# Kernel optimization log

Hardware: AMD Instinct MI355X
Metric: run time of the kernel (lower is better)

The kernel has to match this reference:

```python
import jax, jax.numpy as jnp
import numpy as np

V, D, T, L, H = 32000, 1024, 2048, 2, 16
HS = D // H  # per-head dim (head_size // nheads)
FF = 4 * D
EPS = 1e-5


def _ln(x, g, b):
    m = jnp.mean(x, axis=-1, keepdims=True)
    v = jnp.mean((x - m) ** 2, axis=-1, keepdims=True)
    return (x - m) * jax.lax.rsqrt(v + EPS) * g + b


def setup_inputs() -> dict:
    key = jax.random.key(0)
    ks = jax.random.split(key, 16)
    s = lambda k, shape, fan: jax.random.normal(k, shape, jnp.float32) * (fan ** -0.5)
    return {
        "inputs": jax.random.randint(ks[0], (1, T), 0, V, dtype=jnp.int64),
        "tok_emb": s(ks[1], (V, D), D),
        "pos_emb": s(ks[2], (T, D), D),
        "ln1_g": jnp.ones((L, D)), "ln1_b": jnp.zeros((L, D)),
        "wq": s(ks[3], (L, H, D, HS), D),
        "wk": s(ks[4], (L, H, D, HS), D),
        "wv": s(ks[5], (L, H, D, HS), D),
        "ln2_g": jnp.ones((L, D)), "ln2_b": jnp.zeros((L, D)),
        "w1": s(ks[6], (L, D, FF), D), "b1": jnp.zeros((L, FF)),
        "w2": s(ks[7], (L, FF, D), FF), "b2": jnp.zeros((L, D)),
        "lnf_g": jnp.ones((D,)), "lnf_b": jnp.zeros((D,)),
        "w_un": s(ks[8], (D, V), D), "b_un": jnp.zeros((V,)),
    }


def reference(inputs, tok_emb, pos_emb, ln1_g, ln1_b, wq, wk, wv,
              ln2_g, ln2_b, w1, b1, w2, b2, lnf_g, lnf_b, w_un, b_un):
    b, t = inputs.shape
    x = tok_emb[inputs] + pos_emb[:t]  # [B,T,D]
    mask = jnp.tril(jnp.ones((t, t), dtype=bool))
    scale = jnp.asarray(D, x.dtype) ** -0.5  # source scales by x.shape[-1]**-0.5
    neg_inf = jnp.asarray(-jnp.inf, x.dtype)
    for l in range(L):
        h = _ln(x, ln1_g[l], ln1_b[l])
        q = jnp.einsum('btc,hcs->bhts', h, wq[l])
        k = jnp.einsum('btc,hcs->bhts', h, wk[l])
        v = jnp.einsum('btc,hcs->bhts', h, wv[l])
        scores = jnp.einsum('bhts,bhus->bhtu', q, k) * scale  # [B,H,T,T]
        scores = jnp.where(mask, scores, neg_inf)
        p = jax.nn.softmax(scores, axis=-1)
        att = jnp.einsum('bhtu,bhus->bhts', p, v)  # [B,H,T,HS]
        att = att.transpose(0, 2, 1, 3).reshape(b, t, H * HS)
        x = x + att
        h = _ln(x, ln2_g[l], ln2_b[l])
        h = jax.nn.relu(h @ w1[l] + b1[l]) @ w2[l] + b2[l]
        x = x + h
    x = _ln(x, lnf_g, lnf_b)
    return x @ w_un + b_un  # [B,T,V]
```

## Files before the change

### kernel.cpp

```cpp
#include <hip/hip_runtime.h>
#include <hip/hip_bf16.h>

#define TT 2048
#define DD 1024
#define NH 16
#define HSZ 64
#define FFD 4096
#define VV 32000
#define NL 2

typedef __bf16 bf16x8 __attribute__((ext_vector_type(8)));
typedef float f32x4 __attribute__((ext_vector_type(4)));

__device__ __forceinline__ unsigned short f2bf(float f) {
    unsigned int u = __float_as_uint(f);
    return (unsigned short)((u + 0x7FFFu + ((u >> 16) & 1u)) >> 16);
}

#define GLL(gsrc, ldst) \
  __builtin_amdgcn_global_load_lds((const __attribute__((address_space(1))) void*)(gsrc), \
                                   (__attribute__((address_space(3))) void*)(ldst), 16, 0, 0)

#define SWZ64(L)  ((L) ^ ((((L) >> 7) & 3) << 4))
#define SWZ128(L) ((L) ^ ((((L) >> 7) & 7) << 4))

#define VMW(n) asm volatile("s_waitcnt vmcnt(" #n ")" ::: "memory")

__global__ __launch_bounds__(256) void embed_kernel(
    const int* __restrict__ idx, const float* __restrict__ tok,
    const float* __restrict__ pos, float* __restrict__ x)
{
    int t = blockIdx.x;
    int d4 = threadIdx.x * 4;
    int token = idx[t];
    float4 a = *(const float4*)&tok[(size_t)token * DD + d4];
    float4 p = *(const float4*)&pos[(size_t)t * DD + d4];
    float4 r;
    r.x = a.x + p.x; r.y = a.y + p.y; r.z = a.z + p.z; r.w = a.w + p.w;
    *(float4*)&x[(size_t)t * DD + d4] = r;
}

__global__ __launch_bounds__(256) void ln_kernel(
    const float* __restrict__ x, const float* __restrict__ g,
    const float* __restrict__ b, unsigned short* __restrict__ out)
{
    int t = blockIdx.x;
    int tid = threadIdx.x;
    int d4 = tid * 4;
    float4 xv = *(const float4*)&x[(size_t)t * DD + d4];
    float s  = xv.x + xv.y + xv.z + xv.w;
    float s2 = xv.x*xv.x + xv.y*xv.y + xv.z*xv.z + xv.w*xv.w;
    #pragma unroll
    for (int off = 32; off >= 1; off >>= 1) {
        s  += __shfl_xor(s,  off);
        s2 += __shfl_xor(s2, off);
    }
    __shared__ float ls[4], ls2[4];
    int w = tid >> 6;
    if ((tid & 63) == 0) { ls[w] = s; ls2[w] = s2; }
    __syncthreads();
    float sum  = ls[0] + ls[1] + ls[2] + ls[3];
    float sum2 = ls2[0] + ls2[1] + ls2[2] + ls2[3];
    float mean = sum * (1.0f / DD);
    float var  = sum2 * (1.0f / DD) - mean * mean;
    float r = rsqrtf(var + 1e-5f);
    float4 gv = *(const float4*)&g[d4];
    float4 bv = *(const float4*)&b[d4];
    ushort4 pk;
    pk.x = f2bf((xv.x - mean) * r * gv.x + bv.x);
    pk.y = f2bf((xv.y - mean) * r * gv.y + bv.y);
    pk.z = f2bf((xv.z - mean) * r * gv.z + bv.z);
    pk.w = f2bf((xv.w - mean) * r * gv.w + bv.w);
    *(ushort4*)&out[(size_t)t * DD + d4] = pk;
}

__global__ __launch_bounds__(256) void tcast(
    const float* __restrict__ src, unsigned short* __restrict__ dst,
    int R, int C, size_t sstride, size_t dstride)
{
    __shared__ float tile[64][65];
    const float* s = src + (size_t)blockIdx.z * sstride;
    unsigned short* d = dst + (size_t)blockIdx.z * dstride;
    int c0 = blockIdx.x * 64, r0 = blockIdx.y * 64;
    #pragma unroll
    for (int i = 0; i < 16; ++i) {
        int id = i * 256 + threadIdx.x;
        int rr = id >> 6, cc = id & 63;
        tile[rr][cc] = s[(size_t)(r0 + rr) * C + (c0 + cc)];
    }
    __syncthreads();
    #pragma unroll
    for (int i = 0; i < 16; ++i) {
        int id = i * 256 + threadIdx.x;
        int cc = id >> 6, rr = id & 63;
        d[(size_t)(c0 + cc) * R + (r0 + rr)] = f2bf(tile[rr][cc]);
    }
}

__global__ __launch_bounds__(256) void qkv_tcast(
    const float* __restrict__ wq, const float* __restrict__ wk,
    const float* __restrict__ wv, unsigned short* __restrict__ dst)
{
    __shared__ float tile[64][65];
    int l = blockIdx.z;
    int mat = blockIdx.y >> 4, hh = blockIdx.y & 15;
    const float* s = (mat == 0) ? wq : (mat == 1) ? wk : wv;
    s += (((size_t)l * NH + hh) * DD) * HSZ;
    int r0 = blockIdx.x * 64;
    #pragma unroll
    for (int i = 0; i < 16; ++i) {
        int id = i * 256 + threadIdx.x;
        int rr = id >> 6, cc = id & 63;
        tile[rr][cc] = s[(size_t)(r0 + rr) * HSZ + cc];
    }
    __syncthreads();
    unsigned short* d = dst + (size_t)l * 3072 * DD + ((size_t)mat * DD + hh * HSZ) * DD;
    #pragma unroll
    for (int i = 0; i < 16; ++i) {
        int id = i * 256 + threadIdx.x;
        int cc = id >> 6, rr = id & 63;
        d[(size_t)cc * DD + (r0 + rr)] = f2bf(tile[rr][cc]);
    }
}

template<int EPI, int BN>
__global__ __launch_bounds__(256) void mgemm(
    const unsigned short* __restrict__ A, const unsigned short* __restrict__ Bt,
    const float* __restrict__ bias, void* __restrict__ outp,
    int M, int N, int K)
{
    constexpr int FN = BN / 64 * 2;
    __shared__ unsigned short As[3][128 * 32];
    __shared__ unsigned short Bs[3][BN * 32];
    int tid = threadIdx.x;
    int w = tid >> 6, lane = tid & 63;
    int l15 = lane & 15, l4 = lane >> 4;
    int bm = blockIdx.y * 128, bn = blockIdx.x * BN;
    int wr = (w >> 1) * 64, wc = (w & 1) * (BN / 2);

    f32x4 zz = {0.f, 0.f, 0.f, 0.f};
    f32x4 acc[4][FN];
    #pragma unroll
    for (int m = 0; m < 4; ++m)
        #pragma unroll
        for (int n = 0; n < FN; ++n) acc[m][n] = zz;

    int t16 = tid * 16;
    int lg = SWZ64(t16);
    int srow = lg >> 6;
    int skel = (lg & 63) >> 1;
    const unsigned short* aS0 = A + (size_t)(bm + srow) * K + skel;
    const unsigned short* aS1 = A + (size_t)(bm + 64 + srow) * K + skel;
    const unsigned short* bS0 = Bt + (size_t)(bn + srow) * K + skel;
    const unsigned short* bS1 = Bt + (size_t)(bn + 64 + srow) * K + skel;

    #define STAGE(t, slot) do { int kk_ = (t) * 32; \
        GLL(aS0 + kk_, (char*)As[slot] + w * 1024); \
        GLL(aS1 + kk_, (char*)As[slot] + 4096 + w * 1024); \
        GLL(bS0 + kk_, (char*)Bs[slot] + w * 1024); \
        if (BN == 128) GLL(bS1 + kk_, (char*)Bs[slot] + 4096 + w * 1024); } while (0)

    int aoff[4], boff[FN];
    #pragma unroll
    for (int m = 0; m < 4; ++m)
        aoff[m] = SWZ64((wr + m * 16 + l15) * 64 + l4 * 16);
    #pragma unroll
    for (int n = 0; n < FN; ++n)
        boff[n] = SWZ64((wc + n * 16 + l15) * 64 + l4 * 16);

    int nt = K >> 5;
    STAGE(0, 0);
    STAGE(1, 1);
    STAGE(2, 2);
    int slot = 0;
    for (int t = 0; t < nt; ++t) {
        if (BN == 128) {
            if (t + 2 < nt)      VMW(8);
            else if (t + 1 < nt) VMW(4);
            else                 VMW(0);
        } else {
            if (t + 2 < nt)      VMW(6);
            else if (t + 1 < nt) VMW(3);
            else                 VMW(0);
        }
        __builtin_amdgcn_sched_barrier(0);
        __builtin_amdgcn_s_barrier();
        __builtin_amdgcn_sched_barrier(0);
        bf16x8 af[4], bfr[FN];
        #pragma unroll
        for (int m = 0; m < 4; ++m) af[m] = *(const bf16x8*)((const char*)As[slot] + aoff[m]);
        #pragma unroll
        for (int n = 0; n < FN; ++n) bfr[n] = *(const bf16x8*)((const char*)Bs[slot] + boff[n]);
        #pragma unroll
        for (int m = 0; m < 4; ++m)
            #pragma unroll
            for (int n = 0; n < FN; ++n)
                acc[m][n] = __builtin_amdgcn_mfma_f32_16x16x32_bf16(af[m], bfr[n], acc[m][n], 0, 0, 0);
        __builtin_amdgcn_sched_barrier(0);
        __builtin_amdgcn_s_barrier();
        __builtin_amdgcn_sched_barrier(0);
        if (t + 3 < nt) STAGE(t + 3, slot);
        slot = (slot == 2) ? 0 : slot + 1;
    }
    #undef STAGE

    #pragma unroll
    for (int m = 0; m < 4; ++m) {
        int row0 = bm + wr + m * 16 + l4 * 4;
        #pragma unroll
        for (int n = 0; n < FN; ++n) {
            int col = bn + wc + n * 16 + l15;
            f32x4 v = acc[m][n];
            if (EPI == 0) {
                int mat = col >> 10, hh = (col >> 6) & 15, ss = col & 63;
                unsigned short* base = (unsigned short*)outp + (size_t)mat * ((size_t)NH * TT * HSZ);
                if (mat < 2) {
                    #pragma unroll
                    for (int i = 0; i < 4; ++i)
                        base[((size_t)hh * TT + row0 + i) * HSZ + ss] = f2bf(v[i]);
                } else {
                    ushort4 pk;
                    pk.x = f2bf(v[0]); pk.y = f2bf(v[1]); pk.z = f2bf(v[2]); pk.w = f2bf(v[3]);
                    *(ushort4*)&base[((size_t)hh * HSZ + ss) * TT + row0] = pk;
                }
            } else if (EPI == 1) {
                float bb = bias[col];
                unsigned short* o = (unsigned short*)outp;
                #pragma unroll
                for (int i = 0; i < 4; ++i)
                    o[(size_t)(row0 + i) * FFD + col] = f2bf(fmaxf(v[i] + bb, 0.f));
            } else if (EPI == 2) {
                float bb = bias[col];
                float* xx = (float*)outp;
                #pragma unroll
                for (int i = 0; i < 4; ++i)
                    xx[(size_t)(row0 + i) * DD + col] += v[i] + bb;
            }
        }
    }
}

__global__ __launch_bounds__(512, 2) void mgemm256(
    const unsigned short* __restrict__ A, const unsigned short* __restrict__ Bt,
    const float* __restrict__ bias, float* __restrict__ outp,
    int M, int N, int K)
{
    __shared__ unsigned short As[2][2][128 * 64];
    __shared__ unsigned short Bs[2][2][128 * 64];
    int tid = threadIdx.x;
    int w = tid >> 6, lane = tid & 63;
    int l15 = lane & 15, l4 = lane >> 4;
    int wr = w >> 2, wc = w & 3;
    int bid = blockIdx.x;
    int xcd = bid & 7, j = bid >> 3;
    int mt = j & 7, p = xcd * 16 + (j >> 3);
    if (p >= N / 256) return;
    int bm = mt * 256, bn = p * 256;

    f32x4 zz = {0.f, 0.f, 0.f, 0.f};
    f32x4 acc[8][4];
    #pragma unroll
    for (int m = 0; m < 8; ++m)
        #pragma unroll
        for (int n = 0; n < 4; ++n) acc[m][n] = zz;

    int L0 = w * 1024 + lane * 16;
    int Ls = SWZ128(L0);
    int srow = Ls >> 7;
    int skel = (Ls & 127) >> 1;
    const unsigned short* aS[2], *bS[2];
    aS[0] = A + (size_t)(bm + srow) * K + skel;
    aS[1] = A + (size_t)(bm + 128 + srow) * K + skel;
    bS[0] = Bt + (size_t)(bn + srow) * K + skel;
    bS[1] = Bt + (size_t)(bn + 128 + srow) * K + skel;
    size_t g1 = (size_t)64 * K;

    #define STAGE6(t, buf) do { int kk_ = (t) * 64; \
        GLL(aS[0] + kk_,      (char*)As[buf][0] + w * 1024); \
        GLL(aS[0] + g1 + kk_, (char*)As[buf][0] + 8192 + w * 1024); \
        GLL(aS[1] + kk_,      (char*)As[buf][1] + w * 1024); \
        GLL(aS[1] + g1 + kk_, (char*)As[buf][1] + 8192 + w * 1024); \
        GLL(bS[0] + kk_,      (char*)Bs[buf][0] + w * 1024); \
        GLL(bS[0] + g1 + kk_, (char*)Bs[buf][0] + 8192 + w * 1024); \
        GLL(bS[1] + kk_,      (char*)Bs[buf][1] + w * 1024); \
        GLL(bS[1] + g1 + kk_, (char*)Bs[buf][1] + 8192 + w * 1024); } while (0)

    int aoff[8][2], boff[4][2];
    #pragma unroll
    for (int m = 0; m < 8; ++m)
        #pragma unroll
        for (int ks = 0; ks < 2; ++ks) {
            int La = (m * 16 + l15) * 128 + ks * 64 + l4 * 16;
            aoff[m][ks] = SWZ128(La);
        }
    #pragma unroll
    for (int n = 0; n < 4; ++n)
        #pragma unroll
        for (int ks = 0; ks < 2; ++ks) {
            int Lb = ((wc & 1) * 64 + n * 16 + l15) * 128 + ks * 64 + l4 * 16;
            boff[n][ks] = SWZ128(Lb);
        }

    int nt = K >> 6;
    STAGE6(0, 0);
    STAGE6(1, 1);
    for (int t = 0; t < nt; ++t) {
        int buf = t & 1;
        if (t + 1 < nt) VMW(8);
        else            VMW(0);
        __builtin_amdgcn_sched_barrier(0);
        __builtin_amdgcn_s_barrier();
        __builtin_amdgcn_sched_barrier(0);
        const char* ab = (const char*)As[buf][wr];
        const char* bb = (const char*)Bs[buf][wc >> 1];
        bf16x8 bfr[4][2];
        #pragma unroll
        for (int n = 0; n < 4; ++n)
            #pragma unroll
            for (int ks = 0; ks < 2; ++ks)
                bfr[n][ks] = *(const bf16x8*)(bb + boff[n][ks]);
        __builtin_amdgcn_s_setprio(1);
        #pragma unroll
        for (int rh = 0; rh < 2; ++rh) {
            bf16x8 af[4][2];
            #pragma unroll
            for (int mm = 0; mm < 4; ++mm)
                #pragma unroll
                for (int ks = 0; ks < 2; ++ks)
                    af[mm][ks] = *(const bf16x8*)(ab + aoff[rh * 4 + mm][ks]);
            #pragma unroll
            for (int mm = 0; mm < 4; ++mm)
                #pragma unroll
                for (int n = 0; n < 4; ++n) {
                    acc[rh*4+mm][n] = __builtin_amdgcn_mfma_f32_16x16x32_bf16(af[mm][0], bfr[n][0], acc[rh*4+mm][n], 0, 0, 0);
                    acc[rh*4+mm][n] = __builtin_amdgcn_mfma_f32_16x16x32_bf16(af[mm][1], bfr[n][1], acc[rh*4+mm][n], 0, 0, 0);
                }
        }
        __builtin_amdgcn_s_setprio(0);
        __builtin_amdgcn_sched_barrier(0);
        __builtin_amdgcn_s_barrier();
        __builtin_amdgcn_sched_barrier(0);
        if (t + 2 < nt) STAGE6(t + 2, buf);
    }
    #undef STAGE6

    #pragma unroll
    for (int m = 0; m < 8; ++m) {
        int row0 = bm + wr * 128 + m * 16 + l4 * 4;
        #pragma unroll
        for (int n = 0; n < 4; ++n) {
            int col = bn + wc * 64 + n * 16 + l15;
            float bb = bias[col];
            f32x4 v = acc[m][n];
            #pragma unroll
            for (int i = 0; i < 4; ++i)
                outp[(size_t)(row0 + i) * VV + col] = v[i] + bb;
        }
    }
}

__global__ __launch_bounds__(256) void attn_kernel(
    const unsigned short* __restrict__ qg, const unsigned short* __restrict__ kg,
    const unsigned short* __restrict__ vt, float* __restrict__ x)
{
    __shared__ unsigned short Ks[2][64 * 64];
    __shared__ unsigned short Vs[2][64 * 64];
    __shared__ unsigned short Ps[4][16 * 64];
    int tid = threadIdx.x;
    int w = tid >> 6, lane = tid & 63;
    int l15 = lane & 15, l4 = lane >> 4;
    int hh = blockIdx.y;
    int qb = (31 - blockIdx.x) * 64;

    const unsigned short* qrow = qg + ((size_t)hh * TT + qb + w * 16 + l15) * HSZ + l4 * 8;
    bf16x8 qf0 = *(const bf16x8*)(qrow);
    bf16x8 qf1 = *(const bf16x8*)(qrow + 32);

    int t16 = tid * 16;
    int lgs = SWZ128(t16);
    int surow = lgs >> 7;
    int subyte = lgs & 127;
    const char* kbase = (const char*)(kg + (size_t)hh * TT * HSZ);
    const char* vbase = (const char*)(vt + (size_t)hh * HSZ * TT);

    #define ASTAGE(ib, buf) do { \
        int ub_ = (ib) * 64; \
        GLL(kbase + (size_t)(ub_ + surow) * 128 + subyte,          (char*)Ks[buf] + w * 1024); \
        GLL(kbase + (size_t)(ub_ + 32 + surow) * 128 + subyte,     (char*)Ks[buf] + 4096 + w * 1024); \
        GLL(vbase + (size_t)surow * 4096 + ub_ * 2 + subyte,       (char*)Vs[buf] + w * 1024); \
        GLL(vbase + (size_t)(surow + 32) * 4096 + ub_ * 2 + subyte,(char*)Vs[buf] + 4096 + w * 1024); \
    } while (0)

    f32x4 zz = {0.f, 0.f, 0.f, 0.f};
    f32x4 o[4];
    #pragma unroll
    for (int i = 0; i < 4; ++i) o[i] = zz;
    float mrun = -INFINITY, lrun = 0.f;

    const float scale = 0.03125f;
    int nkv = (qb >> 6) + 1;
    ASTAGE(0, 0);
    if (nkv > 1) ASTAGE(1, 1);
    int cur = 0;
    for (int ib = 0; ib < nkv; ++ib) {
        bool diag = (ib * 64 == qb);
        if (ib + 1 < nkv) VMW(4);
        else              VMW(0);
        __builtin_amdgcn_sched_barrier(0);
        __builtin_amdgcn_s_barrier();
        __builtin_amdgcn_sched_barrier(0);
        const char* ksc = (const char*)Ks[cur];
        const char* vsc = (const char*)Vs[cur];

        f32x4 sfr[4];
        __builtin_amdgcn_s_setprio(1);
        #pragma unroll
        for (int f = 0; f < 4; ++f) {
            int lgb = (f * 16 + l15) * 128 + l4 * 16;
            bf16x8 k0 = *(const bf16x8*)(ksc + SWZ128(lgb));
            bf16x8 k1 = *(const bf16x8*)(ksc + SWZ128(lgb + 64));
            f32x4 z = zz;
            z = __builtin_amdgcn_mfma_f32_16x16x32_bf16(k0, qf0, z, 0, 0, 0);
            z = __builtin_amdgcn_mfma_f32_16x16x32_bf16(k1, qf1, z, 0, 0, 0);
            sfr[f] = z;
        }
        __builtin_amdgcn_s_setprio(0);

        float mx = -INFINITY;
        #pragma unroll
        for (int f = 0; f < 4; ++f)
            #pragma unroll
            for (int i = 0; i < 4; ++i) {
                float s = sfr[f][i] * scale;
                if (diag && (16 * f + (l4 << 2) + i) > (w * 16 + l15)) s = -INFINITY;
                sfr[f][i] = s;
                mx = fmaxf(mx, s);
            }
        mx = fmaxf(mx, __shfl_xor(mx, 16));
        mx = fmaxf(mx, __shfl_xor(mx, 32));
        bool grow = __any(mx > mrun + 8.0f);
        float c = 1.0f;
        if (grow) {
            float mn = fmaxf(mrun, mx);
            c = __expf(mrun - mn);
            mrun = mn;
        }
        float ps = 0.f;
        #pragma unroll
        for (int f = 0; f < 4; ++f)
            #pragma unroll
            for (int i = 0; i < 4; ++i) {
                float p = __expf(sfr[f][i] - mrun);
                sfr[f][i] = p;
                ps += p;
            }
        ps += __shfl_xor(ps, 16);
        ps += __shfl_xor(ps, 32);
        lrun = lrun * c + ps;
        if (grow) {
            #pragma unroll
            for (int i = 0; i < 4; ++i) {
                float ci = __shfl(c, (lane & 48) + (l4 << 2) + i);
                #pragma unroll
                for (int sf = 0; sf < 4; ++sf) o[sf][i] *= ci;
            }
        }

        unsigned short* pw = Ps[w];
        #pragma unroll
        for (int f = 0; f < 4; ++f) {
            unsigned a0 = ((unsigned)f2bf(sfr[f][0])) | (((unsigned)f2bf(sfr[f][1])) << 16);
            unsigned a1 = ((unsigned)f2bf(sfr[f][2])) | (((unsigned)f2bf(sfr[f][3])) << 16);
            int byte0 = l15 * 128 + (16 * f + (l4 << 2)) * 2;
            *(unsigned*)((char*)pw + SWZ128(byte0)) = a0;
            *(unsigned*)((char*)pw + SWZ128(byte0 + 4)) = a1;
        }
        bf16x8 pa0 = *(const bf16x8*)((const char*)pw + SWZ128(l15 * 128 + l4 * 16));
        bf16x8 pa1 = *(const bf16x8*)((const char*)pw + SWZ128(l15 * 128 + 64 + l4 * 16));
        __builtin_amdgcn_s_setprio(1);
        #pragma unroll
        for (int sf = 0; sf < 4; ++sf) {
            int lgb = (sf * 16 + l15) * 128 + l4 * 16;
            bf16x8 v0 = *(const bf16x8*)(vsc + SWZ128(lgb));
            bf16x8 v1 = *(const bf16x8*)(vsc + SWZ128(lgb + 64));
            o[sf] = __builtin_amdgcn_mfma_f32_16x16x32_bf16(pa0, v0, o[sf], 0, 0, 0);
            o[sf] = __builtin_amdgcn_mfma_f32_16x16x32_bf16(pa1, v1, o[sf], 0, 0, 0);
        }
        __builtin_amdgcn_s_setprio(0);
        __builtin_amdgcn_sched_barrier(0);
        __builtin_amdgcn_s_barrier();
        __builtin_amdgcn_sched_barrier(0);
        if (ib + 2 < nkv) ASTAGE(ib + 2, cur);
        cur ^= 1;
    }
    #undef ASTAGE
    float rl[4];
    #pragma unroll
    for (int i = 0; i < 4; ++i)
        rl[i] = 1.0f / __shfl(lrun, (lane & 48) + (l4 << 2) + i);
    #pragma unroll
    for (int sf = 0; sf < 4; ++sf)
        #pragma unroll
        for (int i = 0; i < 4; ++i) {
            int q = qb + w * 16 + l4 * 4 + i;
            int d = hh * HSZ + sf * 16 + l15;
            x[(size_t)q * DD + d] += o[sf][i] * rl[i];
        }
}

extern "C" void kernel_launch(void* const* d_in, const int* in_sizes, int n_in,
                              void* d_out, int out_size, void* d_ws, size_t ws_size,
                              hipStream_t stream)
{
    const int*   idx    = (const int*)  d_in[0];
    const float* tok    = (const float*)d_in[1];
    const float* pos    = (const float*)d_in[2];
    const float* ln1_g  = (const float*)d_in[3];
    const float* ln1_b  = (const float*)d_in[4];
    const float* wq     = (const float*)d_in[5];
    const float* wk     = (const float*)d_in[6];
    const float* wv     = (const float*)d_in[7];
    const float* ln2_g  = (const float*)d_in[8];
    const float* ln2_b  = (const float*)d_in[9];
    const float* w1     = (const float*)d_in[10];
    const float* b1     = (const float*)d_in[11];
    const float* w2     = (const float*)d_in[12];
    const float* b2     = (const float*)d_in[13];
    const float* lnf_g  = (const float*)d_in[14];
    const float* lnf_b  = (const float*)d_in[15];
    const float* w_un   = (const float*)d_in[16];
    const float* b_un   = (const float*)d_in[17];
    float* out = (float*)d_out;

    char* W = (char*)d_ws;
    float*          x    = (float*)(W);
    unsigned short* h    = (unsigned short*)(W + 8388608);
    unsigned short* qg   = (unsigned short*)(W + 12582912);
    unsigned short* kg   = (unsigned short*)(W + 16777216);
    unsigned short* vt   = (unsigned short*)(W + 20971520);
    unsigned short* h1   = (unsigned short*)(W + 25165824);
    unsigned short* wqkvT= (unsigned short*)(W + 41943040);
    unsigned short* w1T  = (unsigned short*)(W + 54525952);
    unsigned short* w2T  = (unsigned short*)(W + 71303168);
    unsigned short* wunT = (unsigned short*)(W + 88080384);
    (void)kg; (void)ws_size; (void)in_sizes; (void)n_in; (void)out_size;

    qkv_tcast<<<dim3(16, 48, 2), 256, 0, stream>>>(wq, wk, wv, wqkvT);
    tcast<<<dim3(64, 16, 2), 256, 0, stream>>>(w1, w1T, DD, FFD, (size_t)DD * FFD, (size_t)DD * FFD);
    tcast<<<dim3(16, 64, 2), 256, 0, stream>>>(w2, w2T, FFD, DD, (size_t)FFD * DD, (size_t)FFD * DD);
    tcast<<<dim3(500, 16, 1), 256, 0, stream>>>(w_un, wunT, DD, VV, 0, 0);

    embed_kernel<<<TT, 256, 0, stream>>>(idx, tok, pos, x);

    for (int l = 0; l < NL; ++l) {
        ln_kernel<<<TT, 256, 0, stream>>>(x, ln1_g + l * DD, ln1_b + l * DD, h);
        mgemm<0, 64><<<dim3(48, 16), 256, 0, stream>>>(h, wqkvT + (size_t)l * 3072 * DD, nullptr, qg, TT, 3072, DD);
        attn_kernel<<<dim3(32, 16), 256, 0, stream>>>(qg, kg, vt, x);
        ln_kernel<<<TT, 256, 0, stream>>>(x, ln2_g + l * DD, ln2_b + l * DD, h);
        mgemm<1, 128><<<dim3(32, 16), 256, 0, stream>>>(h, w1T + (size_t)l * FFD * DD, b1 + (size_t)l * FFD, h1, TT, FFD, DD);
        mgemm<2, 64><<<dim3(16, 16), 256, 0, stream>>>(h1, w2T + (size_t)l * DD * FFD, b2 + (size_t)l * DD, x, TT, DD, FFD);
    }

    ln_kernel<<<TT, 256, 0, stream>>>(x, lnf_g, lnf_b, h);
    mgemm256<<<dim3(1024), 512, 0, stream>>>(h, wunT, b_un, out, TT, VV, DD);
}
```

Before: 658.9 us.

## Split-K the FFN down-projection and load attention K/V directly from global

The second FFN GEMM is split into two K-halves over a z grid dimension. Each half writes a partial fp32 buffer, and a new reduce kernel adds both partials, the bias and the residual into x, so the launch has twice as many blocks. The attention kernel drops its LDS double-buffered K/V staging and block barriers and instead reads K and V fragments straight from global memory, relying on cache hits. It also remaps the 1D grid so heads are spread across XCDs. The split adds extra partial-buffer traffic and a launch, and the direct global loads may expose memory latency that the staging used to hide.

```diff
diff --git a/kernel.cpp b/kernel.cpp
--- a/kernel.cpp
+++ b/kernel.cpp
@@ -127,7 +127,7 @@
 __global__ __launch_bounds__(256) void mgemm(
     const unsigned short* __restrict__ A, const unsigned short* __restrict__ Bt,
     const float* __restrict__ bias, void* __restrict__ outp,
-    int M, int N, int K)
+    int M, int N, int K, int Kst)
 {
     constexpr int FN = BN / 64 * 2;
     __shared__ unsigned short As[3][128 * 32];
@@ -137,6 +137,12 @@
     int l15 = lane & 15, l4 = lane >> 4;
     int bm = blockIdx.y * 128, bn = blockIdx.x * BN;
     int wr = (w >> 1) * 64, wc = (w & 1) * (BN / 2);
+    if (EPI == 3) {
+        int z = blockIdx.z;
+        A  += (size_t)z * K;
+        Bt += (size_t)z * K;
+        outp = (float*)outp + (size_t)z * TT * DD;
+    }
 
     f32x4 zz = {0.f, 0.f, 0.f, 0.f};
     f32x4 acc[4][FN];
@@ -149,10 +155,10 @@
     int lg = SWZ64(t16);
     int srow = lg >> 6;
     int skel = (lg & 63) >> 1;
-    const unsigned short* aS0 = A + (size_t)(bm + srow) * K + skel;
-    const unsigned short* aS1 = A + (size_t)(bm + 64 + srow) * K + skel;
-    const unsigned short* bS0 = Bt + (size_t)(bn + srow) * K + skel;
-    const unsigned short* bS1 = Bt + (size_t)(bn + 64 + srow) * K + skel;
+    const unsigned short* aS0 = A + (size_t)(bm + srow) * Kst + skel;
+    const unsigned short* aS1 = A + (size_t)(bm + 64 + srow) * Kst + skel;
+    const unsigned short* bS0 = Bt + (size_t)(bn + srow) * Kst + skel;
+    const unsigned short* bS1 = Bt + (size_t)(bn + 64 + srow) * Kst + skel;
 
     #define STAGE(t, slot) do { int kk_ = (t) * 32; \
         GLL(aS0 + kk_, (char*)As[slot] + w * 1024); \
@@ -235,9 +241,32 @@
                 #pragma unroll
                 for (int i = 0; i < 4; ++i)
                     xx[(size_t)(row0 + i) * DD + col] += v[i] + bb;
+            } else {
+                float* xx = (float*)outp;
+                #pragma unroll
+                for (int i = 0; i < 4; ++i)
+                    xx[(size_t)(row0 + i) * DD + col] = v[i];
             }
         }
     }
+}
+
+__global__ __launch_bounds__(256) void ffn2_reduce(
+    const float* __restrict__ P, const float* __restrict__ b2,
+    float* __restrict__ x)
+{
+    int t = blockIdx.x;
+    int d4 = threadIdx.x * 4;
+    size_t o = (size_t)t * DD + d4;
+    float4 p0 = *(const float4*)&P[o];
+    float4 p1 = *(const float4*)&P[o + (size_t)TT * DD];
+    float4 bb = *(const float4*)&b2[d4];
+    float4 xv = *(float4*)&x[o];
+    xv.x += p0.x + p1.x + bb.x;
+    xv.y += p0.y + p1.y + bb.y;
+    xv.z += p0.z + p1.z + bb.z;
+    xv.w += p0.w + p1.w + bb.w;
+    *(float4*)&x[o] = xv;
 }
 
 __global__ __launch_bounds__(512, 2) void mgemm256(
@@ -363,34 +392,22 @@
     const unsigned short* __restrict__ qg, const unsigned short* __restrict__ kg,
     const unsigned short* __restrict__ vt, float* __restrict__ x)
 {
-    __shared__ unsigned short Ks[2][64 * 64];
-    __shared__ unsigned short Vs[2][64 * 64];
     __shared__ unsigned short Ps[4][16 * 64];
     int tid = threadIdx.x;
     int w = tid >> 6, lane = tid & 63;
     int l15 = lane & 15, l4 = lane >> 4;
-    int hh = blockIdx.y;
-    int qb = (31 - blockIdx.x) * 64;
+    int bid = blockIdx.x;
+    int j = bid >> 3;
+    int hh = (bid & 7) * 2 + (j & 1);
+    int qb = (31 - (j >> 1)) * 64;
 
     const unsigned short* qrow = qg + ((size_t)hh * TT + qb + w * 16 + l15) * HSZ + l4 * 8;
     bf16x8 qf0 = *(const bf16x8*)(qrow);
     bf16x8 qf1 = *(const bf16x8*)(qrow + 32);
 
-    int t16 = tid * 16;
-    int lgs = SWZ128(t16);
-    int surow = lgs >> 7;
-    int subyte = lgs & 127;
     const char* kbase = (const char*)(kg + (size_t)hh * TT * HSZ);
     const char* vbase = (const char*)(vt + (size_t)hh * HSZ * TT);
 
-    #define ASTAGE(ib, buf) do { \
-        int ub_ = (ib) * 64; \
-        GLL(kbase + (size_t)(ub_ + surow) * 128 + subyte,          (char*)Ks[buf] + w * 1024); \
-        GLL(kbase + (size_t)(ub_ + 32 + surow) * 128 + subyte,     (char*)Ks[buf] + 4096 + w * 1024); \
-        GLL(vbase + (size_t)surow * 4096 + ub_ * 2 + subyte,       (char*)Vs[buf] + w * 1024); \
-        GLL(vbase + (size_t)(surow + 32) * 4096 + ub_ * 2 + subyte,(char*)Vs[buf] + 4096 + w * 1024); \
-    } while (0)
-
     f32x4 zz = {0.f, 0.f, 0.f, 0.f};
     f32x4 o[4];
     #pragma unroll
@@ -399,26 +416,17 @@
 
     const float scale = 0.03125f;
     int nkv = (qb >> 6) + 1;
-    ASTAGE(0, 0);
-    if (nkv > 1) ASTAGE(1, 1);
-    int cur = 0;
     for (int ib = 0; ib < nkv; ++ib) {
-        bool diag = (ib * 64 == qb);
-        if (ib + 1 < nkv) VMW(4);
-        else              VMW(0);
-        __builtin_amdgcn_sched_barrier(0);
-        __builtin_amdgcn_s_barrier();
-        __builtin_amdgcn_sched_barrier(0);
-        const char* ksc = (const char*)Ks[cur];
-        const char* vsc = (const char*)Vs[cur];
+        int ub = ib * 64;
+        bool diag = (ub == qb);
 
         f32x4 sfr[4];
         __builtin_amdgcn_s_setprio(1);
         #pragma unroll
         for (int f = 0; f < 4; ++f) {
-            int lgb = (f * 16 + l15) * 128 + l4 * 16;
-            bf16x8 k0 = *(const bf16x8*)(ksc + SWZ128(lgb));
-            bf16x8 k1 = *(const bf16x8*)(ksc + SWZ128(lgb + 64));
+            const char* krow = kbase + (size_t)(ub + f * 16 + l15) * 128 + l4 * 16;
+            bf16x8 k0 = *(const bf16x8*)(krow);
+            bf16x8 k1 = *(const bf16x8*)(krow + 64);
             f32x4 z = zz;
             z = __builtin_amdgcn_mfma_f32_16x16x32_bf16(k0, qf0, z, 0, 0, 0);
             z = __builtin_amdgcn_mfma_f32_16x16x32_bf16(k1, qf1, z, 0, 0, 0);
@@ -480,20 +488,14 @@
         __builtin_amdgcn_s_setprio(1);
         #pragma unroll
         for (int sf = 0; sf < 4; ++sf) {
-            int lgb = (sf * 16 + l15) * 128 + l4 * 16;
-            bf16x8 v0 = *(const bf16x8*)(vsc + SWZ128(lgb));
-            bf16x8 v1 = *(const bf16x8*)(vsc + SWZ128(lgb + 64));
+            const char* vrow = vbase + (size_t)(sf * 16 + l15) * (TT * 2) + ub * 2 + l4 * 16;
+            bf16x8 v0 = *(const bf16x8*)(vrow);
+            bf16x8 v1 = *(const bf16x8*)(vrow + 64);
             o[sf] = __builtin_amdgcn_mfma_f32_16x16x32_bf16(pa0, v0, o[sf], 0, 0, 0);
             o[sf] = __builtin_amdgcn_mfma_f32_16x16x32_bf16(pa1, v1, o[sf], 0, 0, 0);
         }
         __builtin_amdgcn_s_setprio(0);
-        __builtin_amdgcn_sched_barrier(0);
-        __builtin_amdgcn_s_barrier();
-        __builtin_amdgcn_sched_barrier(0);
-        if (ib + 2 < nkv) ASTAGE(ib + 2, cur);
-        cur ^= 1;
-    }
-    #undef ASTAGE
+    }
     float rl[4];
     #pragma unroll
     for (int i = 0; i < 4; ++i)
@@ -538,6 +540,7 @@
     unsigned short* qg   = (unsigned short*)(W + 12582912);
     unsigned short* kg   = (unsigned short*)(W + 16777216);
     unsigned short* vt   = (unsigned short*)(W + 20971520);
+    float*          Pp   = (float*)(W + 8388608);
     unsigned short* h1   = (unsigned short*)(W + 25165824);
     unsigned short* wqkvT= (unsigned short*)(W + 41943040);
     unsigned short* w1T  = (unsigned short*)(W + 54525952);
@@ -554,11 +557,12 @@
 
     for (int l = 0; l < NL; ++l) {
         ln_kernel<<<TT, 256, 0, stream>>>(x, ln1_g + l * DD, ln1_b + l * DD, h);
-        mgemm<0, 64><<<dim3(48, 16), 256, 0, stream>>>(h, wqkvT + (size_t)l * 3072 * DD, nullptr, qg, TT, 3072, DD);
-        attn_kernel<<<dim3(32, 16), 256, 0, stream>>>(qg, kg, vt, x);
+        mgemm<0, 64><<<dim3(48, 16), 256, 0, stream>>>(h, wqkvT + (size_t)l * 3072 * DD, nullptr, qg, TT, 3072, DD, DD);
+        attn_kernel<<<512, 256, 0, stream>>>(qg, kg, vt, x);
         ln_kernel<<<TT, 256, 0, stream>>>(x, ln2_g + l * DD, ln2_b + l * DD, h);
-        mgemm<1, 128><<<dim3(32, 16), 256, 0, stream>>>(h, w1T + (size_t)l * FFD * DD, b1 + (size_t)l * FFD, h1, TT, FFD, DD);
-        mgemm<2, 64><<<dim3(16, 16), 256, 0, stream>>>(h1, w2T + (size_t)l * DD * FFD, b2 + (size_t)l * DD, x, TT, DD, FFD);
+        mgemm<1, 128><<<dim3(32, 16), 256, 0, stream>>>(h, w1T + (size_t)l * FFD * DD, b1 + (size_t)l * FFD, h1, TT, FFD, DD, DD);
+        mgemm<3, 64><<<dim3(16, 16, 2), 256, 0, stream>>>(h1, w2T + (size_t)l * DD * FFD, nullptr, Pp, TT, DD, FFD / 2, FFD);
+        ffn2_reduce<<<TT, 256, 0, stream>>>(Pp, b2 + (size_t)l * DD, x);
     }
 
     ln_kernel<<<TT, 256, 0, stream>>>(x, lnf_g, lnf_b, h);
```

New measurement: 716.0 us. +8.7%, slower.

## Split-K the FFN down-projection GEMM with a separate reduce kernel

Applied to the files above, without the earlier changes.

The second FFN GEMM (K=4096, only 256 blocks) now runs as a two-way split-K launch. Each z-slice writes fp32 partials to a scratch buffer, and a new reduce kernel adds both partials plus the bias into the residual stream. This doubles the block count to fill more CUs and shortens each block's K loop. In exchange it adds an extra kernel launch and about 16MB of partial-buffer traffic. The scratch buffer reuses workspace starting at the h/qg region, which is assumed dead at that point.

```diff
diff --git a/kernel.cpp b/kernel.cpp
--- a/kernel.cpp
+++ b/kernel.cpp
@@ -127,7 +127,7 @@
 __global__ __launch_bounds__(256) void mgemm(
     const unsigned short* __restrict__ A, const unsigned short* __restrict__ Bt,
     const float* __restrict__ bias, void* __restrict__ outp,
-    int M, int N, int K)
+    int M, int N, int K, int Kst)
 {
     constexpr int FN = BN / 64 * 2;
     __shared__ unsigned short As[3][128 * 32];
@@ -137,6 +137,12 @@
     int l15 = lane & 15, l4 = lane >> 4;
     int bm = blockIdx.y * 128, bn = blockIdx.x * BN;
     int wr = (w >> 1) * 64, wc = (w & 1) * (BN / 2);
+    if (EPI == 3) {
+        int z = blockIdx.z;
+        A  += (size_t)z * K;
+        Bt += (size_t)z * K;
+        outp = (float*)outp + (size_t)z * TT * DD;
+    }
 
     f32x4 zz = {0.f, 0.f, 0.f, 0.f};
     f32x4 acc[4][FN];
@@ -149,10 +155,10 @@
     int lg = SWZ64(t16);
     int srow = lg >> 6;
     int skel = (lg & 63) >> 1;
-    const unsigned short* aS0 = A + (size_t)(bm + srow) * K + skel;
-    const unsigned short* aS1 = A + (size_t)(bm + 64 + srow) * K + skel;
-    const unsigned short* bS0 = Bt + (size_t)(bn + srow) * K + skel;
-    const unsigned short* bS1 = Bt + (size_t)(bn + 64 + srow) * K + skel;
+    const unsigned short* aS0 = A + (size_t)(bm + srow) * Kst + skel;
+    const unsigned short* aS1 = A + (size_t)(bm + 64 + srow) * Kst + skel;
+    const unsigned short* bS0 = Bt + (size_t)(bn + srow) * Kst + skel;
+    const unsigned short* bS1 = Bt + (size_t)(bn + 64 + srow) * Kst + skel;
 
     #define STAGE(t, slot) do { int kk_ = (t) * 32; \
         GLL(aS0 + kk_, (char*)As[slot] + w * 1024); \
@@ -235,9 +241,32 @@
                 #pragma unroll
                 for (int i = 0; i < 4; ++i)
                     xx[(size_t)(row0 + i) * DD + col] += v[i] + bb;
+            } else {
+                float* xx = (float*)outp;
+                #pragma unroll
+                for (int i = 0; i < 4; ++i)
+                    xx[(size_t)(row0 + i) * DD + col] = v[i];
             }
         }
     }
+}
+
+__global__ __launch_bounds__(256) void ffn2_reduce(
+    const float* __restrict__ P, const float* __restrict__ b2,
+    float* __restrict__ x)
+{
+    int t = blockIdx.x;
+    int d4 = threadIdx.x * 4;
+    size_t o = (size_t)t * DD + d4;
+    float4 p0 = *(const float4*)&P[o];
+    float4 p1 = *(const float4*)&P[o + (size_t)TT * DD];
+    float4 bb = *(const float4*)&b2[d4];
+    float4 xv = *(float4*)&x[o];
+    xv.x += p0.x + p1.x + bb.x;
+    xv.y += p0.y + p1.y + bb.y;
+    xv.z += p0.z + p1.z + bb.z;
+    xv.w += p0.w + p1.w + bb.w;
+    *(float4*)&x[o] = xv;
 }
 
 __global__ __launch_bounds__(512, 2) void mgemm256(
@@ -538,6 +567,7 @@
     unsigned short* qg   = (unsigned short*)(W + 12582912);
     unsigned short* kg   = (unsigned short*)(W + 16777216);
     unsigned short* vt   = (unsigned short*)(W + 20971520);
+    float*          Pp   = (float*)(W + 8388608);
     unsigned short* h1   = (unsigned short*)(W + 25165824);
     unsigned short* wqkvT= (unsigned short*)(W + 41943040);
     unsigned short* w1T  = (unsigned short*)(W + 54525952);
@@ -554,11 +584,12 @@
 
     for (int l = 0; l < NL; ++l) {
         ln_kernel<<<TT, 256, 0, stream>>>(x, ln1_g + l * DD, ln1_b + l * DD, h);
-        mgemm<0, 64><<<dim3(48, 16), 256, 0, stream>>>(h, wqkvT + (size_t)l * 3072 * DD, nullptr, qg, TT, 3072, DD);
+        mgemm<0, 64><<<dim3(48, 16), 256, 0, stream>>>(h, wqkvT + (size_t)l * 3072 * DD, nullptr, qg, TT, 3072, DD, DD);
         attn_kernel<<<dim3(32, 16), 256, 0, stream>>>(qg, kg, vt, x);
         ln_kernel<<<TT, 256, 0, stream>>>(x, ln2_g + l * DD, ln2_b + l * DD, h);
-        mgemm<1, 128><<<dim3(32, 16), 256, 0, stream>>>(h, w1T + (size_t)l * FFD * DD, b1 + (size_t)l * FFD, h1, TT, FFD, DD);
-        mgemm<2, 64><<<dim3(16, 16), 256, 0, stream>>>(h1, w2T + (size_t)l * DD * FFD, b2 + (size_t)l * DD, x, TT, DD, FFD);
+        mgemm<1, 128><<<dim3(32, 16), 256, 0, stream>>>(h, w1T + (size_t)l * FFD * DD, b1 + (size_t)l * FFD, h1, TT, FFD, DD, DD);
+        mgemm<3, 64><<<dim3(16, 16, 2), 256, 0, stream>>>(h1, w2T + (size_t)l * DD * FFD, nullptr, Pp, TT, DD, FFD / 2, FFD);
+        ffn2_reduce<<<TT, 256, 0, stream>>>(Pp, b2 + (size_t)l * DD, x);
     }
 
     ln_kernel<<<TT, 256, 0, stream>>>(x, lnf_g, lnf_b, h);
```

Result: faster. 616.1 us (-6.5%).
